# Kernel tuning notes

Hardware: AMD Instinct MI355X
Metric: run time of the kernel (lower is better)

Reference implementation:

```python
import jax, jax.numpy as jnp
import numpy as np
import math

NEG = -1000000.0

def setup_inputs() -> dict:
    key = jax.random.key(0)
    k1, k2, k3, k4 = jax.random.split(key, 4)
    B, S, D = 64, 1024, 64
    query = jax.random.normal(k1, (B, S, D), dtype=jnp.float32)
    key_t = jax.random.normal(k2, (B, S, D), dtype=jnp.float32)
    value = jax.random.normal(k3, (B, S, D), dtype=jnp.float32)
    valid_lens = jax.random.randint(k4, (B,), 1, S + 1, dtype=jnp.int32)
    return {"query": query, "key": key_t, "value": value, "valid_lens": valid_lens}

def reference(query, key, value, valid_lens):
    # query/key/value: [B, S, D]; valid_lens: [B]
    d = query.shape[-1]
    scores = jnp.einsum('bqd,bkd->bqk', query, key) / math.sqrt(d)
    Sk = key.shape[1]
    # 1D valid_lens -> same mask for every query row (repeat_interleave semantics)
    mask = jnp.arange(Sk)[None, None, :] < valid_lens[:, None, None]  # [B,1,Sk]
    scores = jnp.where(mask, scores, NEG)
    weights = jax.nn.softmax(scores, axis=-1)
    # dropout p=0.0 -> identity
    return jnp.einsum('bqk,bkd->bqd', weights, value)
```

## Files before the change

### kernel.cpp

```cpp
#include <hip/hip_runtime.h>
#include <hip/hip_bf16.h>
#include <cstdint>


typedef __attribute__((ext_vector_type(8))) short short8;
typedef __attribute__((ext_vector_type(4))) short short4v;
typedef __attribute__((ext_vector_type(4))) float f32x4;

#define B_   64
#define S_   1024
#define D_   64
#define BQ   64
#define BK   64
#define KPAD 68
#define PPAD 68

__device__ __forceinline__ uint32_t pk2(float a, float b) {
    float2 t; t.x = a; t.y = b;
    union { __hip_bfloat162 h; uint32_t u; } c;
    c.h = __float22bfloat162_rn(t);
    return c.u;
}

__device__ __forceinline__ unsigned short pbf(float f) {
    union { float f; uint32_t u; } v; v.f = f;
    return (unsigned short)((v.u + 0x8000u) >> 16);
}

__device__ __forceinline__ short8 ld8(const unsigned short* p) {
    short4v lo = *(const short4v*)p;
    short4v hi = *(const short4v*)(p + 4);
    return __builtin_shufflevector(lo, hi, 0, 1, 2, 3, 4, 5, 6, 7);
}

__global__ __launch_bounds__(256, 2)
void attn_fwd(const float* __restrict__ Q, const float* __restrict__ K,
              const float* __restrict__ V, const int* __restrict__ VL,
              float* __restrict__ Out) {
    __shared__ unsigned short lK [BK * KPAD];
    __shared__ unsigned short lVt[D_ * 64];
    __shared__ unsigned short lP [4 * 16 * PPAD];

    const int tid  = threadIdx.x;
    const int wave = tid >> 6;
    const int lane = tid & 63;
    const int col  = lane & 15;
    const int quad = lane >> 4;

    const int bid  = blockIdx.x;
    const int b    = (bid & 7) * 8 + (bid >> 7);
    const int q0   = ((bid >> 3) & 15) * BQ;
    const int vlen = VL[b];
    const int ntiles = (vlen + BK - 1) / BK;

    short8 qa[2];
    {
        const int qrow = q0 + wave * 16 + col;
        const float* qp = Q + ((size_t)b * S_ + qrow) * D_ + quad * 8;
        #pragma unroll
        for (int c = 0; c < 2; ++c) {
            float4 x0 = *(const float4*)(qp + c * 32);
            float4 x1 = *(const float4*)(qp + c * 32 + 4);
            union { uint32_t u[4]; short8 s; } qq;
            qq.u[0] = pk2(x0.x, x0.y);
            qq.u[1] = pk2(x0.z, x0.w);
            qq.u[2] = pk2(x1.x, x1.y);
            qq.u[3] = pk2(x1.z, x1.w);
            qa[c] = qq.s;
        }
    }

    f32x4 ofrag[4];
    #pragma unroll
    for (int dt = 0; dt < 4; ++dt) ofrag[dt] = (f32x4){0.f, 0.f, 0.f, 0.f};
    float lsum[4] = {0.f, 0.f, 0.f, 0.f};

    const int r  = tid >> 2;
    const int cc = tid & 3;
    const float* kp0 = K + ((size_t)b * S_ + r) * D_ + cc * 4;
    const float* vp0 = V + ((size_t)b * S_ + r) * D_ + cc * 4;
    const int r3 = (r >> 3) & 1, r4 = (r >> 4) & 1, r5 = (r >> 5) & 1, rlow = r & 7;

    const float cexp = 0.18033688011112042f;

    for (int kt = 0; kt < ntiles; ++kt) {
        const int kbase = kt * BK;
        __syncthreads();

        {
            const float* kp = kp0 + (size_t)kbase * D_;
            const float* vp = vp0 + (size_t)kbase * D_;
            #pragma unroll
            for (int j4 = 0; j4 < 4; ++j4) {
                float4 kx = *(const float4*)(kp + j4 * 16);
                uint2 kv;
                kv.x = pk2(kx.x, kx.y);
                kv.y = pk2(kx.z, kx.w);
                *(uint2*)&lK[r * KPAD + cc * 4 + j4 * 16] = kv;

                float4 vx = *(const float4*)(vp + j4 * 16);
                uint32_t v01 = pk2(vx.x, vx.y);
                uint32_t v23 = pk2(vx.z, vx.w);
                const unsigned short vs[4] = {
                    (unsigned short)v01, (unsigned short)(v01 >> 16),
                    (unsigned short)v23, (unsigned short)(v23 >> 16)};
                const int d4 = j4 & 1, d5 = j4 >> 1;
                const int cb2 = r3 | ((r4 ^ d4) << 1);
                #pragma unroll
                for (int e = 0; e < 4; ++e) {
                    const int d  = cc * 4 + j4 * 16 + e;
                    const int d3 = (cc * 4 + e) >> 3;
                    const int ch = cb2 | (((r5 ^ d5 ^ d3) & 1) << 2);
                    lVt[d * 64 + ch * 8 + rlow] = vs[e];
                }
            }
        }
        __syncthreads();

        f32x4 sfrag[4];
        #pragma unroll
        for (int ct = 0; ct < 4; ++ct) {
            f32x4 acc = (f32x4){0.f, 0.f, 0.f, 0.f};
            #pragma unroll
            for (int c = 0; c < 2; ++c) {
                short8 kb = ld8(&lK[(ct * 16 + col) * KPAD + c * 32 + quad * 8]);
                acc = __builtin_amdgcn_mfma_f32_16x16x32_bf16(qa[c], kb, acc, 0, 0, 0);
            }
            sfrag[ct] = acc;
        }

        unsigned short* pw = &lP[wave * 16 * PPAD];
        if (kbase + BK <= vlen) {
            #pragma unroll
            for (int ct = 0; ct < 4; ++ct)
                #pragma unroll
                for (int rr = 0; rr < 4; ++rr) {
                    float e = exp2f(sfrag[ct][rr] * cexp);
                    lsum[rr] += e;
                    pw[(quad * 4 + rr) * PPAD + ct * 16 + col] = pbf(e);
                }
        } else {
            #pragma unroll
            for (int ct = 0; ct < 4; ++ct) {
                const bool ok = (kbase + ct * 16 + col) < vlen;
                #pragma unroll
                for (int rr = 0; rr < 4; ++rr) {
                    float e = ok ? exp2f(sfrag[ct][rr] * cexp) : 0.0f;
                    lsum[rr] += e;
                    pw[(quad * 4 + rr) * PPAD + ct * 16 + col] = pbf(e);
                }
            }
        }

        #pragma unroll
        for (int kc = 0; kc < 2; ++kc) {
            short8 pa = ld8(&pw[col * PPAD + kc * 32 + quad * 8]);
            #pragma unroll
            for (int dt = 0; dt < 4; ++dt) {
                const int chR = (quad & 1)
                              | ((((quad >> 1) ^ dt) & 1) << 1)
                              | (((kc ^ (dt >> 1) ^ (col >> 3)) & 1) << 2);
                short8 vb = *(const short8*)&lVt[(dt * 16 + col) * 64 + chR * 8];
                ofrag[dt] = __builtin_amdgcn_mfma_f32_16x16x32_bf16(pa, vb, ofrag[dt], 0, 0, 0);
            }
        }
    }

    float inv[4];
    #pragma unroll
    for (int rr = 0; rr < 4; ++rr) {
        float s = lsum[rr];
        #pragma unroll
        for (int m = 1; m < 16; m <<= 1) s += __shfl_xor(s, m, 64);
        inv[rr] = 1.0f / s;
    }
    const int qrow0 = q0 + wave * 16 + quad * 4;
    #pragma unroll
    for (int rr = 0; rr < 4; ++rr) {
        float* op = Out + ((size_t)b * S_ + qrow0 + rr) * D_ + col;
        #pragma unroll
        for (int dt = 0; dt < 4; ++dt)
            op[dt * 16] = ofrag[dt][rr] * inv[rr];
    }
}

extern "C" void kernel_launch(void* const* d_in, const int* in_sizes, int n_in,
                              void* d_out, int out_size, void* d_ws, size_t ws_size,
                              hipStream_t stream) {
    const float* Q  = (const float*)d_in[0];
    const float* K  = (const float*)d_in[1];
    const float* V  = (const float*)d_in[2];
    const int*   VL = (const int*)d_in[3];
    float* Out = (float*)d_out;
    dim3 grid(B_ * (S_ / BQ));
    attn_fwd<<<grid, 256, 0, stream>>>(Q, K, V, VL, Out);
}
```

Measured before the change: 126.0 us.

## Double-buffer K/V tiles with register prefetch and new V-transpose swizzle

The K and V shared-memory tiles become double-buffered. The next tile's global loads are issued into registers before the current tile is computed, which removes one barrier per iteration and overlaps global latency with MFMA work. The V transpose now writes packed 32-bit pairs of adjacent rows under a new XOR swizzle instead of scalar 16-bit stores. The launch bound also goes to 4 blocks/SM and exp2f is replaced by the hardware exp2 builtin. The costs are more LDS per block and more registers held for the prefetch, which may limit occupancy.

```diff
diff --git a/kernel.cpp b/kernel.cpp
--- a/kernel.cpp
+++ b/kernel.cpp
@@ -13,7 +13,6 @@
 #define BQ   64
 #define BK   64
 #define KPAD 68
-#define PPAD 68
 
 __device__ __forceinline__ uint32_t pk2(float a, float b) {
     float2 t; t.x = a; t.y = b;
@@ -21,25 +20,23 @@
     c.h = __float22bfloat162_rn(t);
     return c.u;
 }
-
 __device__ __forceinline__ unsigned short pbf(float f) {
     union { float f; uint32_t u; } v; v.f = f;
     return (unsigned short)((v.u + 0x8000u) >> 16);
 }
-
 __device__ __forceinline__ short8 ld8(const unsigned short* p) {
     short4v lo = *(const short4v*)p;
     short4v hi = *(const short4v*)(p + 4);
     return __builtin_shufflevector(lo, hi, 0, 1, 2, 3, 4, 5, 6, 7);
 }
 
-__global__ __launch_bounds__(256, 2)
+__global__ __launch_bounds__(256, 4)
 void attn_fwd(const float* __restrict__ Q, const float* __restrict__ K,
               const float* __restrict__ V, const int* __restrict__ VL,
               float* __restrict__ Out) {
-    __shared__ unsigned short lK [BK * KPAD];
-    __shared__ unsigned short lVt[D_ * 64];
-    __shared__ unsigned short lP [4 * 16 * PPAD];
+    __shared__ __align__(16) unsigned short lK [2][BK * KPAD];
+    __shared__ __align__(16) unsigned short lVt[2][D_ * 64];
+    __shared__ __align__(16) unsigned short lP [4 * 16 * KPAD];
 
     const int tid  = threadIdx.x;
     const int wave = tid >> 6;
@@ -52,6 +49,26 @@
     const int q0   = ((bid >> 3) & 15) * BQ;
     const int vlen = VL[b];
     const int ntiles = (vlen + BK - 1) / BK;
+
+    const int T  = tid >> 4;
+    const int m  = tid & 15;
+    const int Tl = T & 3;
+    const int cb = T >> 2;
+    const int dcs = m >> 1;
+    const int sws = ((dcs & 1) << 2) | (dcs >> 1);
+
+    const float* Kb = K + (size_t)b * S_ * D_ + 4 * m;
+    const float* Vb = V + (size_t)b * S_ * D_ + 4 * m;
+
+    float4 kr[4], vr[4];
+    {
+        #pragma unroll
+        for (int j = 0; j < 4; ++j) {
+            const int row = 2 * T + (j >> 1) * 32 + (j & 1);
+            kr[j] = *(const float4*)(Kb + (size_t)row * D_);
+            vr[j] = *(const float4*)(Vb + (size_t)row * D_);
+        }
+    }
 
     short8 qa[2];
     {
@@ -75,69 +92,65 @@
     for (int dt = 0; dt < 4; ++dt) ofrag[dt] = (f32x4){0.f, 0.f, 0.f, 0.f};
     float lsum[4] = {0.f, 0.f, 0.f, 0.f};
 
-    const int r  = tid >> 2;
-    const int cc = tid & 3;
-    const float* kp0 = K + ((size_t)b * S_ + r) * D_ + cc * 4;
-    const float* vp0 = V + ((size_t)b * S_ + r) * D_ + cc * 4;
-    const int r3 = (r >> 3) & 1, r4 = (r >> 4) & 1, r5 = (r >> 5) & 1, rlow = r & 7;
-
     const float cexp = 0.18033688011112042f;
 
     for (int kt = 0; kt < ntiles; ++kt) {
+        unsigned short* bK = lK[kt & 1];
+        unsigned short* bV = lVt[kt & 1];
+
+        #pragma unroll
+        for (int j = 0; j < 4; ++j) {
+            const int row = 2 * T + (j >> 1) * 32 + (j & 1);
+            uint2 kv;
+            kv.x = pk2(kr[j].x, kr[j].y);
+            kv.y = pk2(kr[j].z, kr[j].w);
+            *(uint2*)&bK[row * KPAD + 4 * m] = kv;
+        }
+        #pragma unroll
+        for (int i = 0; i < 2; ++i) {
+            const int p = (cb + 4 * i) ^ sws;
+            unsigned short* base = &bV[p * 8 + 2 * Tl];
+            const float4 va = vr[2 * i], vb2 = vr[2 * i + 1];
+            *(uint32_t*)&base[(4 * m + 0) * 64] = pk2(va.x, vb2.x);
+            *(uint32_t*)&base[(4 * m + 1) * 64] = pk2(va.y, vb2.y);
+            *(uint32_t*)&base[(4 * m + 2) * 64] = pk2(va.z, vb2.z);
+            *(uint32_t*)&base[(4 * m + 3) * 64] = pk2(va.w, vb2.w);
+        }
+
+        if (kt + 1 < ntiles) {
+            const size_t off = (size_t)(kt + 1) * BK * D_;
+            #pragma unroll
+            for (int j = 0; j < 4; ++j) {
+                const int row = 2 * T + (j >> 1) * 32 + (j & 1);
+                kr[j] = *(const float4*)(Kb + off + (size_t)row * D_);
+                vr[j] = *(const float4*)(Vb + off + (size_t)row * D_);
+            }
+        }
+
+        __syncthreads();
+
         const int kbase = kt * BK;
-        __syncthreads();
-
-        {
-            const float* kp = kp0 + (size_t)kbase * D_;
-            const float* vp = vp0 + (size_t)kbase * D_;
-            #pragma unroll
-            for (int j4 = 0; j4 < 4; ++j4) {
-                float4 kx = *(const float4*)(kp + j4 * 16);
-                uint2 kv;
-                kv.x = pk2(kx.x, kx.y);
-                kv.y = pk2(kx.z, kx.w);
-                *(uint2*)&lK[r * KPAD + cc * 4 + j4 * 16] = kv;
-
-                float4 vx = *(const float4*)(vp + j4 * 16);
-                uint32_t v01 = pk2(vx.x, vx.y);
-                uint32_t v23 = pk2(vx.z, vx.w);
-                const unsigned short vs[4] = {
-                    (unsigned short)v01, (unsigned short)(v01 >> 16),
-                    (unsigned short)v23, (unsigned short)(v23 >> 16)};
-                const int d4 = j4 & 1, d5 = j4 >> 1;
-                const int cb2 = r3 | ((r4 ^ d4) << 1);
-                #pragma unroll
-                for (int e = 0; e < 4; ++e) {
-                    const int d  = cc * 4 + j4 * 16 + e;
-                    const int d3 = (cc * 4 + e) >> 3;
-                    const int ch = cb2 | (((r5 ^ d5 ^ d3) & 1) << 2);
-                    lVt[d * 64 + ch * 8 + rlow] = vs[e];
-                }
-            }
-        }
-        __syncthreads();
-
         f32x4 sfrag[4];
         #pragma unroll
         for (int ct = 0; ct < 4; ++ct) {
             f32x4 acc = (f32x4){0.f, 0.f, 0.f, 0.f};
             #pragma unroll
             for (int c = 0; c < 2; ++c) {
-                short8 kb = ld8(&lK[(ct * 16 + col) * KPAD + c * 32 + quad * 8]);
-                acc = __builtin_amdgcn_mfma_f32_16x16x32_bf16(qa[c], kb, acc, 0, 0, 0);
+                short8 kb2 = ld8(&bK[(ct * 16 + col) * KPAD + c * 32 + quad * 8]);
+                acc = __builtin_amdgcn_mfma_f32_16x16x32_bf16(qa[c], kb2, acc, 0, 0, 0);
             }
             sfrag[ct] = acc;
         }
 
-        unsigned short* pw = &lP[wave * 16 * PPAD];
+        unsigned short* pw = &lP[wave * 16 * KPAD];
         if (kbase + BK <= vlen) {
             #pragma unroll
             for (int ct = 0; ct < 4; ++ct)
                 #pragma unroll
                 for (int rr = 0; rr < 4; ++rr) {
-                    float e = exp2f(sfrag[ct][rr] * cexp);
+                    float e = __builtin_amdgcn_exp2f(sfrag[ct][rr] * cexp);
                     lsum[rr] += e;
-                    pw[(quad * 4 + rr) * PPAD + ct * 16 + col] = pbf(e);
+                    pw[(quad * 4 + rr) * KPAD + ct * 16 + col] = pbf(e);
                 }
         } else {
             #pragma unroll
@@ -145,22 +158,21 @@
                 const bool ok = (kbase + ct * 16 + col) < vlen;
                 #pragma unroll
                 for (int rr = 0; rr < 4; ++rr) {
-                    float e = ok ? exp2f(sfrag[ct][rr] * cexp) : 0.0f;
+                    float e = ok ? __builtin_amdgcn_exp2f(sfrag[ct][rr] * cexp) : 0.0f;
                     lsum[rr] += e;
-                    pw[(quad * 4 + rr) * PPAD + ct * 16 + col] = pbf(e);
+                    pw[(quad * 4 + rr) * KPAD + ct * 16 + col] = pbf(e);
                 }
             }
         }
 
         #pragma unroll
         for (int kc = 0; kc < 2; ++kc) {
-            short8 pa = ld8(&pw[col * PPAD + kc * 32 + quad * 8]);
+            short8 pa = ld8(&pw[col * KPAD + kc * 32 + quad * 8]);
             #pragma unroll
             for (int dt = 0; dt < 4; ++dt) {
-                const int chR = (quad & 1)
-                              | ((((quad >> 1) ^ dt) & 1) << 1)
-                              | (((kc ^ (dt >> 1) ^ (col >> 3)) & 1) << 2);
-                short8 vb = *(const short8*)&lVt[(dt * 16 + col) * 64 + chR * 8];
+                const int sr = ((col >> 3) << 2) | dt;
+                const int p  = (kc * 4 + quad) ^ sr;
+                short8 vb = *(const short8*)&bV[(dt * 16 + col) * 64 + p * 8];
                 ofrag[dt] = __builtin_amdgcn_mfma_f32_16x16x32_bf16(pa, vb, ofrag[dt], 0, 0, 0);
             }
         }
@@ -171,7 +183,7 @@
     for (int rr = 0; rr < 4; ++rr) {
         float s = lsum[rr];
         #pragma unroll
-        for (int m = 1; m < 16; m <<= 1) s += __shfl_xor(s, m, 64);
+        for (int mm = 1; mm < 16; mm <<= 1) s += __shfl_xor(s, mm, 64);
         inv[rr] = 1.0f / s;
     }
     const int qrow0 = q0 + wave * 16 + quad * 4;
```

Result: faster. 118.1 us (-6.3%).
